# Performance work log

Hardware: AMD Instinct MI355X
Metric: run time of the kernel (lower is better)

The kernel has to match this reference:

```python
import jax, jax.numpy as jnp
import numpy as np

N = 200000
D = 128
PARAM_SCALE = 1.0 / D  # keep exp() exponent bounded (original torch.rand init overflows at scale)


def setup_inputs() -> dict:
    key = jax.random.key(0)
    kx, k1, k2, k3, k4 = jax.random.split(key, 5)
    X = jax.random.normal(kx, (N, D), dtype=jnp.float32)
    W_sum = jax.random.uniform(k1, (D, D), dtype=jnp.float32) * PARAM_SCALE
    W_alpha = jax.random.uniform(k2, (D, D), dtype=jnp.float32) * PARAM_SCALE
    a_alpha = jax.random.uniform(k3, (D, 1), dtype=jnp.float32) * PARAM_SCALE
    b_alpha = jax.random.uniform(k4, (D, 1), dtype=jnp.float32) * PARAM_SCALE
    return {"X": X, "W_sum": W_sum, "W_alpha": W_alpha,
            "a_alpha": a_alpha, "b_alpha": b_alpha}


def reference(X, W_sum, W_alpha, a_alpha, b_alpha):
    # a_w = a_alpha^T @ W_alpha, b_w = b_alpha^T @ W_alpha  -> (D,) each
    a_w = a_alpha[:, 0] @ W_alpha
    b_w = b_alpha[:, 0] @ W_alpha
    # alpha_j = exp(a_w . X[0] + b_w . X[j])  -> (N,)
    alpha = jnp.exp(a_w @ X[0] + X @ b_w)
    # weighted sum over all rows, normalized by sum of (unnormalized) weights
    sum_output = (alpha @ X) / jnp.sum(alpha)  # (D,)
    return sum_output @ W_sum  # (D,)
```

## Files before the change

### kernel.cpp

```cpp
#include <hip/hip_runtime.h>
#include <hip/hip_bf16.h>

#define D 128

__global__ __launch_bounds__(1024) void prep_kernel(
    const float* __restrict__ X,
    const float* __restrict__ W_alpha,
    const float* __restrict__ a_alpha,
    const float* __restrict__ b_alpha,
    float* __restrict__ bw_out,
    float* __restrict__ c_out)
{
    const int t = threadIdx.x;
    const int k = t & 127;
    const int g = t >> 7;

    float aw = 0.f, bw = 0.f;
    #pragma unroll
    for (int i = g * 16; i < g * 16 + 16; ++i) {
        const float w = W_alpha[i * D + k];
        aw = fmaf(a_alpha[i], w, aw);
        bw = fmaf(b_alpha[i], w, bw);
    }
    __shared__ float raw[8][D], rbw[8][D];
    raw[g][k] = aw;
    rbw[g][k] = bw;
    __syncthreads();

    __shared__ float wsum[2];
    if (t < D) {
        float A = 0.f, B = 0.f;
        #pragma unroll
        for (int r = 0; r < 8; ++r) { A += raw[r][t]; B += rbw[r][t]; }
        bw_out[t] = B;
        float part = A * X[t];
        #pragma unroll
        for (int m = 32; m >= 1; m >>= 1) part += __shfl_xor(part, m, 64);
        if ((t & 63) == 0) wsum[t >> 6] = part;
    }
    __syncthreads();
    if (t == 0) c_out[0] = wsum[0] + wsum[1];
}

__global__ __launch_bounds__(256) void main_pass_kernel(
    const float* __restrict__ X,
    const float* __restrict__ bw,
    const float* __restrict__ c_ptr,
    float* __restrict__ partial_wsum,
    float* __restrict__ partial_alpha,
    int nrows)
{
    const int t    = threadIdx.x;
    const int col4 = t & 31;
    const int rg   = t >> 5;

    const float4 bwv = reinterpret_cast<const float4*>(bw)[col4];
    const float  c   = *c_ptr;

    float a0 = 0.f, a1 = 0.f, a2 = 0.f, a3 = 0.f;
    float aacc = 0.f;

    const int ntiles = (nrows + 15) >> 4;
    const float4* __restrict__ X4 = reinterpret_cast<const float4*>(X);

    for (int tile = blockIdx.x; tile < ntiles; tile += gridDim.x) {
        const int r0 = tile * 16 + rg * 2;
        const int r1 = r0 + 1;
        const bool v0 = r0 < nrows, v1 = r1 < nrows;
        float4 x0 = v0 ? X4[(size_t)r0 * 32 + col4] : make_float4(0.f,0.f,0.f,0.f);
        float4 x1 = v1 ? X4[(size_t)r1 * 32 + col4] : make_float4(0.f,0.f,0.f,0.f);

        float d0 = fmaf(x0.x, bwv.x, fmaf(x0.y, bwv.y, fmaf(x0.z, bwv.z, x0.w * bwv.w)));
        float d1 = fmaf(x1.x, bwv.x, fmaf(x1.y, bwv.y, fmaf(x1.z, bwv.z, x1.w * bwv.w)));
        #pragma unroll
        for (int m = 16; m >= 1; m >>= 1) {
            d0 += __shfl_xor(d0, m, 64);
            d1 += __shfl_xor(d1, m, 64);
        }
        const float al0 = v0 ? __expf(d0 + c) : 0.f;
        const float al1 = v1 ? __expf(d1 + c) : 0.f;
        if (col4 == 0) aacc += al0 + al1;
        a0 = fmaf(al0, x0.x, fmaf(al1, x1.x, a0));
        a1 = fmaf(al0, x0.y, fmaf(al1, x1.y, a1));
        a2 = fmaf(al0, x0.z, fmaf(al1, x1.z, a2));
        a3 = fmaf(al0, x0.w, fmaf(al1, x1.w, a3));
    }

    __shared__ float red[8][32][4];
    __shared__ float reda[8];
    red[rg][col4][0] = a0;
    red[rg][col4][1] = a1;
    red[rg][col4][2] = a2;
    red[rg][col4][3] = a3;
    if (col4 == 0) reda[rg] = aacc;
    __syncthreads();

    if (t < D) {
        double s = 0.0;
        #pragma unroll
        for (int r = 0; r < 8; ++r) s += (double)red[r][t >> 2][t & 3];
        partial_wsum[(size_t)blockIdx.x * D + t] = (float)s;
    }
    if (t == 0) {
        double s = 0.0;
        #pragma unroll
        for (int r = 0; r < 8; ++r) s += (double)reda[r];
        partial_alpha[blockIdx.x] = (float)s;
    }
}

__global__ __launch_bounds__(512) void reduce1_kernel(
    const float* __restrict__ partial_wsum,
    const float* __restrict__ partial_alpha,
    double* __restrict__ mid,
    double* __restrict__ mida,
    int NB, int NB2)
{
    const int b  = blockIdx.x;
    const int t  = threadIdx.x;
    const int k  = t & 127;
    const int rs = t >> 7;
    const int nper = NB / NB2;

    double s = 0.0;
    for (int j = rs; j < nper; j += 4)
        s += (double)partial_wsum[(size_t)(b + NB2 * j) * D + k];
    __shared__ double red[4][D];
    red[rs][k] = s;

    __shared__ double reda[64];
    if (t < nper && t < 64) {
        double sa = 0.0;
        for (int j = t; j < nper; j += 64) sa += (double)partial_alpha[b + NB2 * j];
        reda[t] = sa;
    }
    __syncthreads();

    if (t < D)
        mid[(size_t)b * D + t] = red[0][t] + red[1][t] + red[2][t] + red[3][t];
    if (t == 0) {
        double sa = 0.0;
        const int lim = nper < 64 ? nper : 64;
        for (int i = 0; i < lim; ++i) sa += reda[i];
        mida[b] = sa;
    }
}

__global__ __launch_bounds__(1024) void final_kernel(
    const double* __restrict__ mid,
    const double* __restrict__ mida,
    const float* __restrict__ W_sum,
    float* __restrict__ out,
    int NB2)
{
    const int t = threadIdx.x;
    const int k = t & 127;
    const int g = t >> 7;

    double ws = 0.0;
    for (int j = g; j < NB2; j += 8)
        ws += mid[(size_t)j * D + k];
    __shared__ double red[8][D];
    red[g][k] = ws;

    __shared__ double reda[64];
    if (t < NB2) reda[t] = mida[t];
    __syncthreads();
    __shared__ double asum_sh;
    if (t == 0) {
        double a = 0.0;
        for (int i = 0; i < NB2; ++i) a += reda[i];
        asum_sh = a;
    }
    __syncthreads();

    __shared__ float s_sh[D];
    if (t < D) {
        double s = 0.0;
        #pragma unroll
        for (int r = 0; r < 8; ++r) s += red[r][t];
        s_sh[t] = (float)(s / asum_sh);
    }
    __syncthreads();

    float o = 0.f;
    #pragma unroll
    for (int kk = g * 16; kk < g * 16 + 16; ++kk)
        o = fmaf(s_sh[kk], W_sum[kk * D + k], o);
    __shared__ float rout[8][D];
    rout[g][k] = o;
    __syncthreads();
    if (t < D) {
        float s = 0.f;
        #pragma unroll
        for (int r = 0; r < 8; ++r) s += rout[r][t];
        out[t] = s;
    }
}

extern "C" void kernel_launch(void* const* d_in, const int* in_sizes, int n_in,
                              void* d_out, int out_size, void* d_ws, size_t ws_size,
                              hipStream_t stream) {
    const float* X       = (const float*)d_in[0];
    const float* W_sum   = (const float*)d_in[1];
    const float* W_alpha = (const float*)d_in[2];
    const float* a_alpha = (const float*)d_in[3];
    const float* b_alpha = (const float*)d_in[4];
    float* out = (float*)d_out;

    const int nrows = in_sizes[0] / D;
    const int NB2 = 64;

    int NB = 2048;
    auto need = [&](int nb) {
        return (size_t)nb * D * sizeof(float)
             + (size_t)nb * sizeof(float)
             + (size_t)NB2 * D * sizeof(double)
             + (size_t)NB2 * sizeof(double)
             + (D + 1) * sizeof(float) + 256;
    };
    while (NB > NB2 && need(NB) > ws_size) NB >>= 1;

    char* ws = (char*)d_ws;
    float*  partial_wsum  = (float*)ws;
    float*  partial_alpha = (float*)(ws + (size_t)NB * D * sizeof(float));
    double* mid           = (double*)(ws + (size_t)NB * D * sizeof(float)
                                         + (size_t)NB * sizeof(float) + 248 - ((size_t)NB * (D + 1) * sizeof(float) + 248) % 8);
    size_t off = (size_t)NB * (D + 1) * sizeof(float);
    off = (off + 255) & ~(size_t)255;
    mid = (double*)(ws + off);
    double* mida = mid + (size_t)NB2 * D;
    float*  bw   = (float*)(mida + NB2);
    float*  cv   = bw + D;

    prep_kernel<<<1, 1024, 0, stream>>>(X, W_alpha, a_alpha, b_alpha, bw, cv);
    main_pass_kernel<<<NB, 256, 0, stream>>>(X, bw, cv, partial_wsum,
                                             partial_alpha, nrows);
    reduce1_kernel<<<NB2, 512, 0, stream>>>(partial_wsum, partial_alpha,
                                            mid, mida, NB, NB2);
    final_kernel<<<1, 1024, 0, stream>>>(mid, mida, W_sum, out, NB2);
}
```

Before: 35.93 us.

## Fuse prep into main pass kernel and prefetch next tile rows

```diff
diff --git a/kernel.cpp b/kernel.cpp
--- a/kernel.cpp
+++ b/kernel.cpp
@@ -3,72 +3,85 @@
 
 #define D 128
 
-__global__ __launch_bounds__(1024) void prep_kernel(
+__global__ __launch_bounds__(256, 8) void fused_main_kernel(
     const float* __restrict__ X,
     const float* __restrict__ W_alpha,
     const float* __restrict__ a_alpha,
     const float* __restrict__ b_alpha,
-    float* __restrict__ bw_out,
-    float* __restrict__ c_out)
-{
-    const int t = threadIdx.x;
-    const int k = t & 127;
-    const int g = t >> 7;
-
-    float aw = 0.f, bw = 0.f;
-    #pragma unroll
-    for (int i = g * 16; i < g * 16 + 16; ++i) {
-        const float w = W_alpha[i * D + k];
-        aw = fmaf(a_alpha[i], w, aw);
-        bw = fmaf(b_alpha[i], w, bw);
-    }
-    __shared__ float raw[8][D], rbw[8][D];
-    raw[g][k] = aw;
-    rbw[g][k] = bw;
-    __syncthreads();
-
-    __shared__ float wsum[2];
-    if (t < D) {
-        float A = 0.f, B = 0.f;
-        #pragma unroll
-        for (int r = 0; r < 8; ++r) { A += raw[r][t]; B += rbw[r][t]; }
-        bw_out[t] = B;
-        float part = A * X[t];
-        #pragma unroll
-        for (int m = 32; m >= 1; m >>= 1) part += __shfl_xor(part, m, 64);
-        if ((t & 63) == 0) wsum[t >> 6] = part;
-    }
-    __syncthreads();
-    if (t == 0) c_out[0] = wsum[0] + wsum[1];
-}
-
-__global__ __launch_bounds__(256) void main_pass_kernel(
-    const float* __restrict__ X,
-    const float* __restrict__ bw,
-    const float* __restrict__ c_ptr,
     float* __restrict__ partial_wsum,
     float* __restrict__ partial_alpha,
     int nrows)
 {
-    const int t    = threadIdx.x;
+    const int t = threadIdx.x;
+
+    __shared__ float aal[D], bal[D];
+    __shared__ float raw2[2][D], rbw2[2][D];
+    __shared__ float bw_sh[D];
+    __shared__ float csum[2];
+
+    if (t < D) { aal[t] = a_alpha[t]; bal[t] = b_alpha[t]; }
+    __syncthreads();
+
+    {
+        const int kk = t & 127;
+        const int gg = t >> 7;
+        float aw = 0.f, bw = 0.f;
+        #pragma unroll 8
+        for (int i = gg * 64; i < gg * 64 + 64; ++i) {
+            const float w = W_alpha[i * D + kk];
+            aw = fmaf(aal[i], w, aw);
+            bw = fmaf(bal[i], w, bw);
+        }
+        raw2[gg][kk] = aw;
+        rbw2[gg][kk] = bw;
+    }
+    __syncthreads();
+
+    if (t < D) {
+        const float A = raw2[0][t] + raw2[1][t];
+        bw_sh[t]      = rbw2[0][t] + rbw2[1][t];
+        float part = A * X[t];
+        #pragma unroll
+        for (int m = 32; m >= 1; m >>= 1) part += __shfl_xor(part, m, 64);
+        if ((t & 63) == 0) csum[t >> 6] = part;
+    }
+    __syncthreads();
+
+    const float c = csum[0] + csum[1];
+
     const int col4 = t & 31;
     const int rg   = t >> 5;
 
-    const float4 bwv = reinterpret_cast<const float4*>(bw)[col4];
-    const float  c   = *c_ptr;
+    const float4 bwv = make_float4(bw_sh[col4 * 4 + 0], bw_sh[col4 * 4 + 1],
+                                   bw_sh[col4 * 4 + 2], bw_sh[col4 * 4 + 3]);
 
     float a0 = 0.f, a1 = 0.f, a2 = 0.f, a3 = 0.f;
     float aacc = 0.f;
 
     const int ntiles = (nrows + 15) >> 4;
     const float4* __restrict__ X4 = reinterpret_cast<const float4*>(X);
-
-    for (int tile = blockIdx.x; tile < ntiles; tile += gridDim.x) {
+    const float4 fz = make_float4(0.f, 0.f, 0.f, 0.f);
+
+    int tile = blockIdx.x;
+    float4 x0 = fz, x1 = fz;
+    bool v0 = false, v1 = false;
+    if (tile < ntiles) {
         const int r0 = tile * 16 + rg * 2;
-        const int r1 = r0 + 1;
-        const bool v0 = r0 < nrows, v1 = r1 < nrows;
-        float4 x0 = v0 ? X4[(size_t)r0 * 32 + col4] : make_float4(0.f,0.f,0.f,0.f);
-        float4 x1 = v1 ? X4[(size_t)r1 * 32 + col4] : make_float4(0.f,0.f,0.f,0.f);
+        v0 = r0 < nrows; v1 = (r0 + 1) < nrows;
+        if (v0) x0 = X4[(size_t)r0 * 32 + col4];
+        if (v1) x1 = X4[(size_t)(r0 + 1) * 32 + col4];
+    }
+
+    while (tile < ntiles) {
+        const int ntile = tile + gridDim.x;
+        float4 n0 = fz, n1 = fz;
+        bool w0 = false, w1 = false;
+        if (ntile < ntiles) {
+            const int r0 = ntile * 16 + rg * 2;
+            w0 = r0 < nrows; w1 = (r0 + 1) < nrows;
+            if (w0) n0 = X4[(size_t)r0 * 32 + col4];
+            if (w1) n1 = X4[(size_t)(r0 + 1) * 32 + col4];
+        }
 
         float d0 = fmaf(x0.x, bwv.x, fmaf(x0.y, bwv.y, fmaf(x0.z, bwv.z, x0.w * bwv.w)));
         float d1 = fmaf(x1.x, bwv.x, fmaf(x1.y, bwv.y, fmaf(x1.z, bwv.z, x1.w * bwv.w)));
@@ -84,6 +97,9 @@
         a1 = fmaf(al0, x0.y, fmaf(al1, x1.y, a1));
         a2 = fmaf(al0, x0.z, fmaf(al1, x1.z, a2));
         a3 = fmaf(al0, x0.w, fmaf(al1, x1.w, a3));
+
+        x0 = n0; x1 = n1; v0 = w0; v1 = w1;
+        tile = ntile;
     }
 
     __shared__ float red[8][32][4];
@@ -215,27 +231,22 @@
     auto need = [&](int nb) {
         return (size_t)nb * D * sizeof(float)
              + (size_t)nb * sizeof(float)
+             + 256
              + (size_t)NB2 * D * sizeof(double)
-             + (size_t)NB2 * sizeof(double)
-             + (D + 1) * sizeof(float) + 256;
+             + (size_t)NB2 * sizeof(double);
     };
     while (NB > NB2 && need(NB) > ws_size) NB >>= 1;
 
     char* ws = (char*)d_ws;
     float*  partial_wsum  = (float*)ws;
     float*  partial_alpha = (float*)(ws + (size_t)NB * D * sizeof(float));
-    double* mid           = (double*)(ws + (size_t)NB * D * sizeof(float)
-                                         + (size_t)NB * sizeof(float) + 248 - ((size_t)NB * (D + 1) * sizeof(float) + 248) % 8);
     size_t off = (size_t)NB * (D + 1) * sizeof(float);
     off = (off + 255) & ~(size_t)255;
-    mid = (double*)(ws + off);
+    double* mid  = (double*)(ws + off);
     double* mida = mid + (size_t)NB2 * D;
-    float*  bw   = (float*)(mida + NB2);
-    float*  cv   = bw + D;
-
-    prep_kernel<<<1, 1024, 0, stream>>>(X, W_alpha, a_alpha, b_alpha, bw, cv);
-    main_pass_kernel<<<NB, 256, 0, stream>>>(X, bw, cv, partial_wsum,
-                                             partial_alpha, nrows);
+
+    fused_main_kernel<<<NB, 256, 0, stream>>>(X, W_alpha, a_alpha, b_alpha,
+                                              partial_wsum, partial_alpha, nrows);
     reduce1_kernel<<<NB2, 512, 0, stream>>>(partial_wsum, partial_alpha,
                                             mid, mida, NB, NB2);
     final_kernel<<<1, 1024, 0, stream>>>(mid, mida, W_sum, out, NB2);
```

Result: no change. 36.11 us (+0.5%).

## Drop cancelling exp constant, prefetch next tile, use float intermediates

Applied to the files above, without the earlier changes.

```diff
diff --git a/kernel.cpp b/kernel.cpp
--- a/kernel.cpp
+++ b/kernel.cpp
@@ -3,49 +3,38 @@
 
 #define D 128
 
+
 __global__ __launch_bounds__(1024) void prep_kernel(
-    const float* __restrict__ X,
     const float* __restrict__ W_alpha,
-    const float* __restrict__ a_alpha,
     const float* __restrict__ b_alpha,
-    float* __restrict__ bw_out,
-    float* __restrict__ c_out)
+    float* __restrict__ bw_out)
 {
     const int t = threadIdx.x;
     const int k = t & 127;
     const int g = t >> 7;
-
-    float aw = 0.f, bw = 0.f;
+    __shared__ float bal[D];
+    if (t < D) bal[t] = b_alpha[t];
+    __syncthreads();
+
+    float bw = 0.f;
     #pragma unroll
-    for (int i = g * 16; i < g * 16 + 16; ++i) {
-        const float w = W_alpha[i * D + k];
-        aw = fmaf(a_alpha[i], w, aw);
-        bw = fmaf(b_alpha[i], w, bw);
-    }
-    __shared__ float raw[8][D], rbw[8][D];
-    raw[g][k] = aw;
+    for (int i = g * 16; i < g * 16 + 16; ++i)
+        bw = fmaf(bal[i], W_alpha[i * D + k], bw);
+
+    __shared__ float rbw[8][D];
     rbw[g][k] = bw;
     __syncthreads();
-
-    __shared__ float wsum[2];
-    if (t < D) {
-        float A = 0.f, B = 0.f;
-        #pragma unroll
-        for (int r = 0; r < 8; ++r) { A += raw[r][t]; B += rbw[r][t]; }
+    if (t < D) {
+        float B = 0.f;
+        #pragma unroll
+        for (int r = 0; r < 8; ++r) B += rbw[r][t];
         bw_out[t] = B;
-        float part = A * X[t];
-        #pragma unroll
-        for (int m = 32; m >= 1; m >>= 1) part += __shfl_xor(part, m, 64);
-        if ((t & 63) == 0) wsum[t >> 6] = part;
-    }
-    __syncthreads();
-    if (t == 0) c_out[0] = wsum[0] + wsum[1];
-}
-
-__global__ __launch_bounds__(256) void main_pass_kernel(
+    }
+}
+
+__global__ __launch_bounds__(256, 8) void main_pass_kernel(
     const float* __restrict__ X,
     const float* __restrict__ bw,
-    const float* __restrict__ c_ptr,
     float* __restrict__ partial_wsum,
     float* __restrict__ partial_alpha,
     int nrows)
@@ -55,20 +44,25 @@
     const int rg   = t >> 5;
 
     const float4 bwv = reinterpret_cast<const float4*>(bw)[col4];
-    const float  c   = *c_ptr;
 
     float a0 = 0.f, a1 = 0.f, a2 = 0.f, a3 = 0.f;
     float aacc = 0.f;
 
-    const int ntiles = (nrows + 15) >> 4;
+    const int ftiles = nrows >> 4;
     const float4* __restrict__ X4 = reinterpret_cast<const float4*>(X);
 
-    for (int tile = blockIdx.x; tile < ntiles; tile += gridDim.x) {
-        const int r0 = tile * 16 + rg * 2;
-        const int r1 = r0 + 1;
-        const bool v0 = r0 < nrows, v1 = r1 < nrows;
-        float4 x0 = v0 ? X4[(size_t)r0 * 32 + col4] : make_float4(0.f,0.f,0.f,0.f);
-        float4 x1 = v1 ? X4[(size_t)r1 * 32 + col4] : make_float4(0.f,0.f,0.f,0.f);
+    int tile = blockIdx.x;
+    size_t addr = ((size_t)blockIdx.x * 16 + rg * 2) * 32 + col4;
+    const size_t step = (size_t)gridDim.x * 512;
+
+    float4 x0, x1;
+    if (tile < ftiles) { x0 = X4[addr]; x1 = X4[addr + 32]; }
+
+    while (tile < ftiles) {
+        const int ntile = tile + gridDim.x;
+        const size_t naddr = addr + (ntile < ftiles ? step : (size_t)0);
+        const float4 n0 = X4[naddr];
+        const float4 n1 = X4[naddr + 32];
 
         float d0 = fmaf(x0.x, bwv.x, fmaf(x0.y, bwv.y, fmaf(x0.z, bwv.z, x0.w * bwv.w)));
         float d1 = fmaf(x1.x, bwv.x, fmaf(x1.y, bwv.y, fmaf(x1.z, bwv.z, x1.w * bwv.w)));
@@ -77,13 +71,40 @@
             d0 += __shfl_xor(d0, m, 64);
             d1 += __shfl_xor(d1, m, 64);
         }
-        const float al0 = v0 ? __expf(d0 + c) : 0.f;
-        const float al1 = v1 ? __expf(d1 + c) : 0.f;
-        if (col4 == 0) aacc += al0 + al1;
+        const float al0 = __expf(d0);
+        const float al1 = __expf(d1);
+        aacc += al0 + al1;
         a0 = fmaf(al0, x0.x, fmaf(al1, x1.x, a0));
         a1 = fmaf(al0, x0.y, fmaf(al1, x1.y, a1));
         a2 = fmaf(al0, x0.z, fmaf(al1, x1.z, a2));
         a3 = fmaf(al0, x0.w, fmaf(al1, x1.w, a3));
+
+        x0 = n0; x1 = n1; addr = naddr; tile = ntile;
+    }
+
+    const int rem = nrows & 15;
+    if (rem && blockIdx.x == 0) {
+        const int r0 = (nrows & ~15) + rg * 2;
+        if (r0 < nrows) {
+            const float4 x0r = X4[(size_t)r0 * 32 + col4];
+            const bool v1 = (r0 + 1) < nrows;
+            const float4 x1r = v1 ? X4[(size_t)(r0 + 1) * 32 + col4]
+                                  : make_float4(0.f, 0.f, 0.f, 0.f);
+            float d0 = fmaf(x0r.x, bwv.x, fmaf(x0r.y, bwv.y, fmaf(x0r.z, bwv.z, x0r.w * bwv.w)));
+            float d1 = fmaf(x1r.x, bwv.x, fmaf(x1r.y, bwv.y, fmaf(x1r.z, bwv.z, x1r.w * bwv.w)));
+            #pragma unroll
+            for (int m = 16; m >= 1; m >>= 1) {
+                d0 += __shfl_xor(d0, m, 64);
+                d1 += __shfl_xor(d1, m, 64);
+            }
+            const float al0 = __expf(d0);
+            const float al1 = v1 ? __expf(d1) : 0.f;
+            aacc += al0 + al1;
+            a0 = fmaf(al0, x0r.x, fmaf(al1, x1r.x, a0));
+            a1 = fmaf(al0, x0r.y, fmaf(al1, x1r.y, a1));
+            a2 = fmaf(al0, x0r.z, fmaf(al1, x1r.z, a2));
+            a3 = fmaf(al0, x0r.w, fmaf(al1, x1r.w, a3));
+        }
     }
 
     __shared__ float red[8][32][4];
@@ -112,8 +133,8 @@
 __global__ __launch_bounds__(512) void reduce1_kernel(
     const float* __restrict__ partial_wsum,
     const float* __restrict__ partial_alpha,
-    double* __restrict__ mid,
-    double* __restrict__ mida,
+    float* __restrict__ mid,
+    float* __restrict__ mida,
     int NB, int NB2)
 {
     const int b  = blockIdx.x;
@@ -129,7 +150,7 @@
     red[rs][k] = s;
 
     __shared__ double reda[64];
-    if (t < nper && t < 64) {
+    if (t < 64) {
         double sa = 0.0;
         for (int j = t; j < nper; j += 64) sa += (double)partial_alpha[b + NB2 * j];
         reda[t] = sa;
@@ -137,18 +158,18 @@
     __syncthreads();
 
     if (t < D)
-        mid[(size_t)b * D + t] = red[0][t] + red[1][t] + red[2][t] + red[3][t];
+        mid[(size_t)b * D + t] = (float)(red[0][t] + red[1][t] + red[2][t] + red[3][t]);
     if (t == 0) {
         double sa = 0.0;
         const int lim = nper < 64 ? nper : 64;
         for (int i = 0; i < lim; ++i) sa += reda[i];
-        mida[b] = sa;
+        mida[b] = (float)sa;
     }
 }
 
 __global__ __launch_bounds__(1024) void final_kernel(
-    const double* __restrict__ mid,
-    const double* __restrict__ mida,
+    const float* __restrict__ mid,
+    const float* __restrict__ mida,
     const float* __restrict__ W_sum,
     float* __restrict__ out,
     int NB2)
@@ -157,19 +178,31 @@
     const int k = t & 127;
     const int g = t >> 7;
 
-    double ws = 0.0;
-    for (int j = g; j < NB2; j += 8)
-        ws += mid[(size_t)j * D + k];
-    __shared__ double red[8][D];
+    const float4* __restrict__ W4 = reinterpret_cast<const float4*>(W_sum);
+    float4 w0 = W4[t], w1 = W4[t + 1024], w2 = W4[t + 2048], w3 = W4[t + 3072];
+
+    __shared__ float red[8][D];
+    float ws = 0.f;
+    #pragma unroll
+    for (int j = 0; j < 8; ++j) {
+        const int row = g + j * 8;
+        if (row < NB2) ws += mid[(size_t)row * D + k];
+    }
     red[g][k] = ws;
 
-    __shared__ double reda[64];
-    if (t < NB2) reda[t] = mida[t];
-    __syncthreads();
+    __shared__ float reda[64];
+    if (t < 64) reda[t] = (t < NB2) ? mida[t] : 0.f;
+
+    __shared__ float wls[D * D];
+    float4* wls4 = reinterpret_cast<float4*>(wls);
+    wls4[t] = w0; wls4[t + 1024] = w1; wls4[t + 2048] = w2; wls4[t + 3072] = w3;
+    __syncthreads();
+
     __shared__ double asum_sh;
     if (t == 0) {
         double a = 0.0;
-        for (int i = 0; i < NB2; ++i) a += reda[i];
+        #pragma unroll
+        for (int i = 0; i < 64; ++i) a += (double)reda[i];
         asum_sh = a;
     }
     __syncthreads();
@@ -178,7 +211,7 @@
     if (t < D) {
         double s = 0.0;
         #pragma unroll
-        for (int r = 0; r < 8; ++r) s += red[r][t];
+        for (int r = 0; r < 8; ++r) s += (double)red[r][t];
         s_sh[t] = (float)(s / asum_sh);
     }
     __syncthreads();
@@ -186,7 +219,7 @@
     float o = 0.f;
     #pragma unroll
     for (int kk = g * 16; kk < g * 16 + 16; ++kk)
-        o = fmaf(s_sh[kk], W_sum[kk * D + k], o);
+        o = fmaf(s_sh[kk], wls[kk * D + k], o);
     __shared__ float rout[8][D];
     rout[g][k] = o;
     __syncthreads();
@@ -204,7 +237,6 @@
     const float* X       = (const float*)d_in[0];
     const float* W_sum   = (const float*)d_in[1];
     const float* W_alpha = (const float*)d_in[2];
-    const float* a_alpha = (const float*)d_in[3];
     const float* b_alpha = (const float*)d_in[4];
     float* out = (float*)d_out;
 
@@ -213,28 +245,24 @@
 
     int NB = 2048;
     auto need = [&](int nb) {
-        return (size_t)nb * D * sizeof(float)
-             + (size_t)nb * sizeof(float)
-             + (size_t)NB2 * D * sizeof(double)
-             + (size_t)NB2 * sizeof(double)
-             + (D + 1) * sizeof(float) + 256;
+        return (size_t)nb * (D + 1) * sizeof(float)
+             + 256
+             + (size_t)NB2 * (D + 1) * sizeof(float)
+             + (D + 8) * sizeof(float);
     };
     while (NB > NB2 && need(NB) > ws_size) NB >>= 1;
 
     char* ws = (char*)d_ws;
-    float*  partial_wsum  = (float*)ws;
-    float*  partial_alpha = (float*)(ws + (size_t)NB * D * sizeof(float));
-    double* mid           = (double*)(ws + (size_t)NB * D * sizeof(float)
-                                         + (size_t)NB * sizeof(float) + 248 - ((size_t)NB * (D + 1) * sizeof(float) + 248) % 8);
+    float* partial_wsum  = (float*)ws;
+    float* partial_alpha = (float*)(ws + (size_t)NB * D * sizeof(float));
     size_t off = (size_t)NB * (D + 1) * sizeof(float);
     off = (off + 255) & ~(size_t)255;
-    mid = (double*)(ws + off);
-    double* mida = mid + (size_t)NB2 * D;
-    float*  bw   = (float*)(mida + NB2);
-    float*  cv   = bw + D;
-
-    prep_kernel<<<1, 1024, 0, stream>>>(X, W_alpha, a_alpha, b_alpha, bw, cv);
-    main_pass_kernel<<<NB, 256, 0, stream>>>(X, bw, cv, partial_wsum,
+    float* mid  = (float*)(ws + off);
+    float* mida = mid + (size_t)NB2 * D;
+    float* bw   = mida + NB2;
+
+    prep_kernel<<<1, 1024, 0, stream>>>(W_alpha, b_alpha, bw);
+    main_pass_kernel<<<NB, 256, 0, stream>>>(X, bw, partial_wsum,
                                              partial_alpha, nrows);
     reduce1_kernel<<<NB2, 512, 0, stream>>>(partial_wsum, partial_alpha,
                                             mid, mida, NB, NB2);
```

After: 36.44 us. No clear change (+1.4%).
